# Kernel optimization log

Measured on AMD Instinct MI355X. Metric: run time of the kernel, lower is better.

The kernel has to match this reference:

```python
import jax, jax.numpy as jnp
import numpy as np

B, C, H, W = 8, 512, 32, 32
S, E = 77, 768
NH = 8
HD = C // NH
HID = 4 * C
EPS2D = 1e-6
EPS_QK = 1.1920929e-07  # torch nn.RMSNorm default eps = fp32 machine eps


def rotate_half(x):
    p = x.reshape(*x.shape[:-1], -1, 2)
    p = jnp.stack([-p[..., 1], p[..., 0]], axis=-1)
    return p.reshape(x.shape)


def rope_1d(x):
    # x: [B, NH, S, HD] -- standard 1D RoPE over the sequence axis
    d = x.shape[-1]
    inv_freq = 1.0 / (10000.0 ** (jnp.arange(0, d, 2, dtype=jnp.float32) / d))
    ang = jnp.arange(x.shape[-2], dtype=jnp.float32)[:, None] * inv_freq[None, :]  # [S, HD/2]
    cos = jnp.repeat(jnp.cos(ang), 2, axis=-1)
    sin = jnp.repeat(jnp.sin(ang), 2, axis=-1)
    return x * cos + rotate_half(x) * sin


def rope_2d(x, freqs, h, w):
    # x: [B, NH, H*W, HD]; freqs: [HD/2, 2] learned (theta_y, theta_x)
    gy, gx = jnp.meshgrid(jnp.arange(h, dtype=jnp.float32), jnp.arange(w, dtype=jnp.float32), indexing='ij')
    ang = gy.reshape(-1)[:, None] * freqs[None, :, 0] + gx.reshape(-1)[:, None] * freqs[None, :, 1]  # [HW, HD/2]
    cos = jnp.repeat(jnp.cos(ang), 2, axis=-1)
    sin = jnp.repeat(jnp.sin(ang), 2, axis=-1)
    return x * cos + rotate_half(x) * sin


def rmsnorm_last(x, wgt, eps):
    return x * jax.lax.rsqrt(jnp.mean(x * x, axis=-1, keepdims=True) + eps) * wgt


def rmsnorm_2d(x, wgt):
    # x: [B,C,H,W], RMS over channel dim (dim=1)
    return x * jax.lax.rsqrt(jnp.mean(x * x, axis=1, keepdims=True) + EPS2D) * wgt[None, :, None, None]


def setup_inputs() -> dict:
    key = jax.random.key(0)
    ks = jax.random.split(key, 12)

    def n(k, shp, s=0.02):
        return jax.random.normal(k, shp, jnp.float32) * s

    return {
        'x': jax.random.normal(ks[0], (B, C, H, W), jnp.float32),
        'cond_seq': jax.random.normal(ks[1], (B, S, E), jnp.float32),
        'final_emb': jax.random.normal(ks[2], (B, E), jnp.float32),
        'mod_w': n(ks[3], (E, 6 * C)),
        'mod_b': jnp.zeros((6 * C,), jnp.float32),
        'norm1_scale': jnp.ones((C,), jnp.float32),
        'norm2_scale': jnp.ones((C,), jnp.float32),
        'qkv_s_w': n(ks[4], (3 * C, C)),
        'qkv_c_w': n(ks[5], (3 * C, E)),
        'rope_freqs': jax.random.normal(ks[6], (HD // 2, 2), jnp.float32),
        'qn_w': jnp.ones((HD,), jnp.float32),
        'kn_w': jnp.ones((HD,), jnp.float32),
        'out_w': n(ks[7], (C, C)),
        'out_b': jnp.zeros((C,), jnp.float32),
        'mlp_w1': n(ks[8], (HID, C)),
        'mlp_b1': jnp.zeros((HID,), jnp.float32),
        'mlp_w2': n(ks[9], (C, HID)),
        'mlp_b2': jnp.zeros((C,), jnp.float32),
    }


def reference(x, cond_seq, final_emb, mod_w, mod_b, norm1_scale, norm2_scale,
              qkv_s_w, qkv_c_w, rope_freqs, qn_w, kn_w, out_w, out_b,
              mlp_w1, mlp_b1, mlp_w2, mlp_b2):
    b, c, h, w = x.shape
    hw = h * w
    # adaLN modulation (Modulation: SiLU -> Linear -> 6 chunks)
    mod = jax.nn.silu(final_emb) @ mod_w + mod_b  # [B, 6C]
    sh1, sc1, g1, sh2, sc2, g2 = jnp.split(mod, 6, axis=-1)

    def modulate(z, shift, scale):
        return z * (1.0 + scale[:, :, None, None]) + shift[:, :, None, None]

    h_mod = modulate(rmsnorm_2d(x, norm1_scale), sh1, sc1)

    # --- FusedAttentionBlock: dual-stream (spatial + conditional) attention ---
    hm = h_mod.reshape(b, c, hw)
    qkv_s = jnp.einsum('bcn,oc->bon', hm, qkv_s_w)  # 1x1 conv, [B,3C,HW]
    q_s, k_s, v_s = jnp.split(qkv_s, 3, axis=1)

    def to_heads(t):  # [B,C,HW] -> [B,NH,HW,HD] (head-major channel layout)
        return t.reshape(b, NH, HD, hw).transpose(0, 1, 3, 2)

    q_s, k_s, v_s = to_heads(q_s), to_heads(k_s), to_heads(v_s)

    qkv_c = jnp.einsum('bse,oe->bso', cond_seq, qkv_c_w)
    qkv_c = qkv_c.reshape(b, -1, 3, NH, HD).transpose(2, 0, 3, 1, 4)
    q_c, k_c, v_c = qkv_c[0], qkv_c[1], qkv_c[2]  # [B,NH,S,HD]

    q = jnp.concatenate([rope_2d(q_s, rope_freqs, h, w), rope_1d(q_c)], axis=2)
    k = jnp.concatenate([rope_2d(k_s, rope_freqs, h, w), rope_1d(k_c)], axis=2)
    v = jnp.concatenate([v_s, v_c], axis=2)

    q = rmsnorm_last(q, qn_w, EPS_QK)
    k = rmsnorm_last(k, kn_w, EPS_QK)

    scale = 1.0 / (HD ** 0.5)
    logits = jnp.einsum('bhqd,bhkd->bhqk', q, k) * scale
    attn = jax.nn.softmax(logits, axis=-1)
    o = jnp.einsum('bhqk,bhkd->bhqd', attn, v)[:, :, :hw, :]  # spatial stream only
    o = o.transpose(0, 2, 1, 3).reshape(b, hw, c)
    o = jnp.einsum('bnc,oc->bno', o, out_w) + out_b
    attn_out = o.transpose(0, 2, 1).reshape(b, c, h, w)

    x = x + g1[:, :, None, None] * attn_out

    # --- MLP (1x1 convs, tanh-approx GELU) ---
    h2 = modulate(rmsnorm_2d(x, norm2_scale), sh2, sc2)
    m = jnp.einsum('bchw,oc->bohw', h2, mlp_w1) + mlp_b1[None, :, None, None]
    m = jax.nn.gelu(m, approximate=True)
    m = jnp.einsum('bchw,oc->bohw', m, mlp_w2) + mlp_b2[None, :, None, None]
    return x + g2[:, :, None, None] * m
```

## Files before the change

kernel.cpp:

```cpp
#include <hip/hip_runtime.h>

constexpr int BATCH = 8, CH = 512, HWN = 1024, SEQ = 77, EMB = 768;
constexpr int NHEAD = 8, HDIM = 64, HIDDEN = 2048, TTOT = 1101;
constexpr int VSTRIDE = 1152;

typedef short bhalf8 __attribute__((ext_vector_type(8)));
typedef float f32x4 __attribute__((ext_vector_type(4)));

__device__ __forceinline__ unsigned short f2bf(float f) {
    unsigned u = __builtin_bit_cast(unsigned, f);
    unsigned r = (u + 0x7fffu + ((u >> 16) & 1u)) >> 16;
    return (unsigned short)r;
}
__device__ __forceinline__ unsigned cvtpk(float a, float b) {
    unsigned r;
    asm("v_cvt_pk_bf16_f32 %0, %1, %2" : "=v"(r) : "v"(a), "v"(b));
    return r;
}
__device__ __forceinline__ float gelu_tanh(float v) {
    float c = v * v * v;
    float t = tanhf(0.7978845608028654f * (v + 0.044715f * c));
    return 0.5f * v * (1.0f + t);
}
__device__ __forceinline__ int swz(int b) { return b ^ ((b >> 3) & 0x70); }

__device__ __forceinline__ void gload16(const void* g, void* l) {
    __builtin_amdgcn_global_load_lds(
        (const __attribute__((address_space(1))) unsigned int*)g,
        (__attribute__((address_space(3))) unsigned int*)l, 16, 0, 0);
}

struct PrepArgs {
    const float* src[6];
    unsigned short* dst[6];
    int n[6];
    const float* freqs;
    float* ct;
    const float* emb;
    const float* mbias;
    float* mod;
    float* se;
    const float* qn;
    const float* kn;
    float* mbound;
};
__global__ void k_prep(PrepArgs a) {
    int y = blockIdx.y;
    int bx = blockIdx.x;
    int tid = threadIdx.x;
    if (y < 6) {
        int i = (bx * 256 + tid) * 4;
        if (i >= a.n[y]) return;
        float4 v = *(const float4*)&a.src[y][i];
        ushort4 o = {f2bf(v.x), f2bf(v.y), f2bf(v.z), f2bf(v.w)};
        *(ushort4*)&a.dst[y][i] = o;
    } else if (y == 6) {
        int i = bx * 256 + tid;
        if (i >= TTOT * 32) return;
        int t = i >> 5, j = i & 31;
        float ang;
        if (t < HWN) {
            ang = (float)(t >> 5) * a.freqs[2 * j] + (float)(t & 31) * a.freqs[2 * j + 1];
        } else {
            float inv = expf(-(float)j * (9.210340371976184f / 32.0f));
            ang = (float)(t - HWN) * inv;
        }
        a.ct[i * 2] = cosf(ang);
        a.ct[i * 2 + 1] = sinf(ang);
    } else {
        if (bx < 24) {
            int i = bx * 1024 + tid * 4;
            int j = i - (i / (6 * CH)) * (6 * CH);
            *(float4*)&a.mod[i] = *(const float4*)&a.mbias[j];
        } else if (bx == 24) {
            if (tid < 64) {
                float mq = fabsf(a.qn[tid]), mk = fabsf(a.kn[tid]);
                #pragma unroll
                for (int o = 1; o < 64; o <<= 1) {
                    mq = fmaxf(mq, __shfl_xor(mq, o));
                    mk = fmaxf(mk, __shfl_xor(mk, o));
                }
                if (tid == 0) a.mbound[0] = 64.0f * mq * mk * 0.18033688011112042f + 1.0f;
            }
        } else if (bx >= 32 && bx < 38) {
            int i = (bx - 32) * 1024 + tid * 4;
            float4 v = *(const float4*)&a.emb[i];
            float4 o;
            o.x = v.x / (1.0f + expf(-v.x));
            o.y = v.y / (1.0f + expf(-v.y));
            o.z = v.z / (1.0f + expf(-v.z));
            o.w = v.w / (1.0f + expf(-v.w));
            *(float4*)&a.se[i] = o;
        }
    }
}

__global__ __launch_bounds__(256) void k_mod(const float* __restrict__ se,
        const float* __restrict__ w, float* __restrict__ mod) {
    int jb = blockIdx.x, b = blockIdx.y, ec = blockIdx.z;
    int j = jb * 256 + threadIdx.x;
    const float* sb = se + b * EMB + ec * 96;
    const float* wb = w + (size_t)(ec * 96) * (6 * CH) + j;
    float acc = 0.f;
    #pragma unroll 8
    for (int e = 0; e < 96; ++e) acc = fmaf(sb[e], wb[(size_t)e * (6 * CH)], acc);
    atomicAdd(&mod[b * (6 * CH) + j], acc);
}

__global__ __launch_bounds__(256) void k_rms2d_mod_t(const float* __restrict__ xin,
        const float* __restrict__ sw, const float* __restrict__ mod, int shoff, int scoff,
        unsigned short* __restrict__ outp) {
    __shared__ float part[4][64];
    __shared__ float rinv[64];
    int b = blockIdx.y;
    int n0 = blockIdx.x * 64;
    int tid = threadIdx.x;
    const float* xb = xin + (size_t)b * CH * HWN;
    {
        int n = n0 + (tid & 63);
        int cg = tid >> 6;
        float ss = 0.f;
        #pragma unroll 8
        for (int c = cg * 128; c < cg * 128 + 128; ++c) {
            float v = xb[(size_t)c * HWN + n];
            ss = fmaf(v, v, ss);
        }
        part[cg][tid & 63] = ss;
    }
    __syncthreads();
    if (tid < 64) {
        float s = part[0][tid] + part[1][tid] + part[2][tid] + part[3][tid];
        rinv[tid] = rsqrtf(s * (1.0f / CH) + 1e-6f);
    }
    __syncthreads();
    int n = n0 + (tid >> 2);
    int cq = tid & 3;
    float r = rinv[tid >> 2];
    const float* mb = mod + b * (6 * CH);
    unsigned short* orow = outp + ((size_t)(b * HWN + n)) * CH;
    for (int jc = 0; jc < 16; ++jc) {
        int c = cq * 128 + jc * 8;
        bhalf8 o;
        #pragma unroll
        for (int u = 0; u < 8; ++u) {
            int cc = c + u;
            float v = xb[(size_t)cc * HWN + n];
            float y = v * r * sw[cc] * (1.0f + mb[scoff + cc]) + mb[shoff + cc];
            o[u] = (short)f2bf(y);
        }
        *(bhalf8*)&orow[c] = o;
    }
}

template <int EPI, int BM, int BN>
__global__ __launch_bounds__(256) void k_gemm_mfma(
        const unsigned short* __restrict__ A, const unsigned short* __restrict__ Bt,
        void* __restrict__ OutV, int M, int N, int K,
        const float* __restrict__ bias, const float* __restrict__ gate,
        const float* __restrict__ res) {
    constexpr int WM = BM / 2, WN = BN / 2;
    constexpr int MI = WM / 16, NI = WN / 16;
    constexpr int CA = BM / 8, CB = BN / 8, CW = (CA + CB) / 4;
    constexpr int BUF = (BM + BN) * 128;
    __shared__ __align__(1024) char SM[2 * BUF];
    int tid = threadIdx.x;
    int w = tid >> 6, l = tid & 63, lg = l >> 4, ll = l & 15;
    int wr = w >> 1, wc = w & 1;
    int m0 = blockIdx.y * BM, n0 = blockIdx.x * BN;
    int r8 = l >> 3, c16 = (l & 7) * 16;
    f32x4 acc[MI][NI] = {};
    const char* Ac = (const char*)A;
    const char* Bc = (const char*)Bt;
    size_t rowBytes = (size_t)K * 2;
    int nt = K >> 6;

    auto stage = [&](int t, int bsel) {
        char* As = SM + bsel * BUF;
        char* Bs = As + BM * 128;
        int k0 = t * 64;
        #pragma unroll
        for (int i = 0; i < CW; ++i) {
            int c = w * CW + i;
            if (c < CA) {
                int row = c * 8 + r8;
                int off = c16 ^ ((row & 7) << 4);
                int ar = m0 + row;
                if (ar > M - 1) ar = M - 1;
                gload16(Ac + (size_t)ar * rowBytes + k0 * 2 + off, As + c * 1024);
            } else {
                int cc = c - CA;
                int row = cc * 8 + r8;
                int off = c16 ^ ((row & 7) << 4);
                gload16(Bc + (size_t)(n0 + row) * rowBytes + k0 * 2 + off, Bs + cc * 1024);
            }
        }
    };
    stage(0, 0);
    __syncthreads();
    for (int t = 0; t < nt; ++t) {
        int cur = t & 1;
        if (t + 1 < nt) stage(t + 1, cur ^ 1);
        char* As = SM + cur * BUF;
        char* Bs = As + BM * 128;
        #pragma unroll
        for (int ks = 0; ks < 2; ++ks) {
            bhalf8 af[MI], bf[NI];
            #pragma unroll
            for (int mi = 0; mi < MI; ++mi)
                af[mi] = *(const bhalf8*)(As + swz((wr * WM + mi * 16 + ll) * 128 + ks * 64 + lg * 16));
            #pragma unroll
            for (int ni = 0; ni < NI; ++ni)
                bf[ni] = *(const bhalf8*)(Bs + swz((wc * WN + ni * 16 + ll) * 128 + ks * 64 + lg * 16));
            __builtin_amdgcn_s_setprio(1);
            #pragma unroll
            for (int mi = 0; mi < MI; ++mi)
                #pragma unroll
                for (int ni = 0; ni < NI; ++ni)
                    acc[mi][ni] = __builtin_amdgcn_mfma_f32_16x16x32_bf16(af[mi], bf[ni], acc[mi][ni], 0, 0, 0);
            __builtin_amdgcn_s_setprio(0);
        }
        __syncthreads();
    }
    if (EPI == 2) {
        unsigned short* Out = (unsigned short*)OutV;
        #pragma unroll
        for (int mi = 0; mi < MI; ++mi)
            #pragma unroll
            for (int ni = 0; ni < NI; ++ni) {
                int col = n0 + wc * WN + ni * 16 + ll;
                float bv = bias[col];
                #pragma unroll
                for (int r = 0; r < 4; ++r) {
                    int mrow = m0 + wr * WM + mi * 16 + 4 * lg + r;
                    Out[(size_t)mrow * N + col] = f2bf(gelu_tanh(acc[mi][ni][r] + bv));
                }
            }
    } else {
        float* Out = (float*)OutV;
        int bidx = m0 >> 10;
        int hw0 = m0 & 1023;
        const float* resb = res + (size_t)bidx * N * HWN;
        float* outb_ = Out + (size_t)bidx * N * HWN;
        #pragma unroll
        for (int ni = 0; ni < NI; ++ni) {
            int ch = n0 + wc * WN + ni * 16 + ll;
            float g = gate[bidx * (6 * CH) + ch];
            float bv = bias[ch];
            #pragma unroll
            for (int mi = 0; mi < MI; ++mi) {
                int t = hw0 + wr * WM + mi * 16 + 4 * lg;
                float4 r4 = *(const float4*)&resb[(size_t)ch * HWN + t];
                f32x4 a = acc[mi][ni];
                float4 o;
                o.x = r4.x + g * (a[0] + bv);
                o.y = r4.y + g * (a[1] + bv);
                o.z = r4.z + g * (a[2] + bv);
                o.w = r4.w + g * (a[3] + bv);
                *(float4*)&outb_[(size_t)ch * HWN + t] = o;
            }
        }
    }
}

template <int COND>
__global__ __launch_bounds__(256) void k_gemm_qkv(
        const unsigned short* __restrict__ A, const unsigned short* __restrict__ Bt,
        int M, int K, int nOff, const float* __restrict__ ct,
        const float* __restrict__ qn, const float* __restrict__ kn,
        unsigned short* __restrict__ qb, unsigned short* __restrict__ kb,
        unsigned short* __restrict__ vT) {
    __shared__ __align__(1024) char SMEM[34816];
    unsigned short* As = (unsigned short*)SMEM;
    unsigned short* Bs = (unsigned short*)(SMEM + 16384);
    int tid = threadIdx.x;
    int w = tid >> 6, l = tid & 63, lg = l >> 4, ll = l & 15;
    int wr = w >> 1, wc = w & 1;
    int m0 = blockIdx.y * 128, n0 = nOff + blockIdx.x * 128;
    int r8 = l >> 3, c16 = (l & 7) * 16;
    f32x4 acc[4][4] = {};
    const char* Ac = (const char*)A;
    const char* Bc = (const char*)Bt;
    size_t rowBytes = (size_t)K * 2;
    for (int k0 = 0; k0 < K; k0 += 64) {
        __syncthreads();
        #pragma unroll
        for (int i = 0; i < 8; ++i) {
            int c = w * 8 + i;
            if (c < 16) {
                int row = c * 8 + r8;
                int off = c16 ^ ((row & 7) << 4);
                int ar = m0 + row;
                if (ar > M - 1) ar = M - 1;
                gload16(Ac + (size_t)ar * rowBytes + k0 * 2 + off, (char*)As + c * 1024);
            } else {
                int cc = c - 16;
                int row = cc * 8 + r8;
                int off = c16 ^ ((row & 7) << 4);
                gload16(Bc + (size_t)(n0 + row) * rowBytes + k0 * 2 + off, (char*)Bs + cc * 1024);
            }
        }
        __syncthreads();
        #pragma unroll
        for (int ks = 0; ks < 2; ++ks) {
            bhalf8 af[4], bf[4];
            #pragma unroll
            for (int mi = 0; mi < 4; ++mi)
                af[mi] = *(const bhalf8*)((char*)As + swz((wr * 64 + mi * 16 + ll) * 128 + ks * 64 + lg * 16));
            #pragma unroll
            for (int ni = 0; ni < 4; ++ni)
                bf[ni] = *(const bhalf8*)((char*)Bs + swz((wc * 64 + ni * 16 + ll) * 128 + ks * 64 + lg * 16));
            __builtin_amdgcn_s_setprio(1);
            #pragma unroll
            for (int mi = 0; mi < 4; ++mi)
                #pragma unroll
                for (int ni = 0; ni < 4; ++ni)
                    acc[mi][ni] = __builtin_amdgcn_mfma_f32_16x16x32_bf16(af[mi], bf[ni], acc[mi][ni], 0, 0, 0);
            __builtin_amdgcn_s_setprio(0);
        }
    }
    int type = n0 >> 9;
    const float2* ct2 = (const float2*)ct;

    if (type >= 2) {
        int hd = (n0 - 1024 + wc * 64) >> 6;
        #pragma unroll
        for (int ni = 0; ni < 4; ++ni) {
            int d = ni * 16 + ll;
            #pragma unroll
            for (int mi = 0; mi < 4; ++mi) {
                int rowL = m0 + wr * 64 + mi * 16 + 4 * lg;
                if (COND == 0) {
                    int b = rowL >> 10, t = rowL & 1023;
                    uint2 pk = {cvtpk(acc[mi][ni][0], acc[mi][ni][1]),
                                cvtpk(acc[mi][ni][2], acc[mi][ni][3])};
                    *(uint2*)&vT[((size_t)(b * 8 + hd) * 64 + d) * VSTRIDE + t] = pk;
                } else {
                    #pragma unroll
                    for (int r = 0; r < 4; ++r) {
                        int row = rowL + r;
                        if (row < M) {
                            int b = row / 77, s = row - b * 77;
                            vT[((size_t)(b * 8 + hd) * 64 + d) * VSTRIDE + 1024 + s] =
                                f2bf(acc[mi][ni][r]);
                        }
                    }
                }
            }
        }
        return;
    }
    const float* wnt = (type == 0) ? qn : kn;
    float wn[4];
    int jj[4];
    #pragma unroll
    for (int ni = 0; ni < 4; ++ni) {
        wn[ni] = wnt[ni * 16 + ll];
        jj[ni] = (ni * 16 + ll) >> 1;
    }
    float sgn = (ll & 1) ? 1.f : -1.f;
    #pragma unroll
    for (int mi = 0; mi < 4; ++mi) {
        int rowL = m0 + wr * 64 + mi * 16 + 4 * lg;
        int tt[4];
        #pragma unroll
        for (int r = 0; r < 4; ++r) {
            if (COND == 0) tt[r] = (rowL + r) & 1023;
            else {
                int row = rowL + r;
                if (row > M - 1) row = M - 1;
                int b = row / 77;
                tt[r] = 1024 + (row - b * 77);
            }
        }
        #pragma unroll
        for (int ni = 0; ni < 4; ++ni) {
            f32x4 a = acc[mi][ni], p;
            #pragma unroll
            for (int r = 0; r < 4; ++r) p[r] = __shfl_xor(a[r], 1);
            #pragma unroll
            for (int r = 0; r < 4; ++r) {
                float2 cs = ct2[tt[r] * 32 + jj[ni]];
                a[r] = fmaf(sgn * p[r], cs.y, a[r] * cs.x);
            }
            acc[mi][ni] = a;
        }
        f32x4 ss = {};
        #pragma unroll
        for (int ni = 0; ni < 4; ++ni)
            #pragma unroll
            for (int r = 0; r < 4; ++r) ss[r] = fmaf(acc[mi][ni][r], acc[mi][ni][r], ss[r]);
        #pragma unroll
        for (int msk = 1; msk < 16; msk <<= 1)
            #pragma unroll
            for (int r = 0; r < 4; ++r) ss[r] += __shfl_xor(ss[r], msk);
        f32x4 ri;
        #pragma unroll
        for (int r = 0; r < 4; ++r) {
            ri[r] = rsqrtf(ss[r] * (1.0f / 64.f) + 1.1920929e-07f);
            if (type == 0) ri[r] *= 0.18033688011112042f;
        }
        #pragma unroll
        for (int ni = 0; ni < 4; ++ni)
            #pragma unroll
            for (int r = 0; r < 4; ++r) acc[mi][ni][r] *= ri[r] * wn[ni];
    }
    __syncthreads();
    unsigned short* stg = (unsigned short*)SMEM;
    #pragma unroll
    for (int mi = 0; mi < 4; ++mi)
        #pragma unroll
        for (int ni = 0; ni < 4; ++ni) {
            int colL = wc * 64 + ni * 16 + ll;
            int rowL = wr * 64 + mi * 16 + 4 * lg;
            #pragma unroll
            for (int r = 0; r < 4; ++r)
                stg[(rowL + r) * 136 + colL] = f2bf(acc[mi][ni][r]);
        }
    __syncthreads();
    int rowO = tid >> 1, half = tid & 1;
    int rowG = m0 + rowO;
    if (COND == 1 && rowG >= M) return;
    int ch0 = n0 + half * 64;
    int b, t;
    if (COND == 0) { b = rowG >> 10; t = rowG & 1023; }
    else { b = rowG / 77; t = 1024 + (rowG - b * 77); }
    unsigned short* dst;
    if (type == 0) dst = qb + ((size_t)(b * 8 + (ch0 >> 6)) * HWN + t) * 64;
    else dst = kb + ((size_t)(b * 8 + ((ch0 - 512) >> 6)) * TTOT + t) * 64;
    #pragma unroll
    for (int i = 0; i < 8; ++i)
        *(bhalf8*)&dst[i * 8] = *(const bhalf8*)&stg[rowO * 136 + half * 64 + i * 8];
}

__global__ __launch_bounds__(256) void k_attn_v7(const unsigned short* __restrict__ qb,
        const unsigned short* __restrict__ kbuf, const unsigned short* __restrict__ vT,
        unsigned short* __restrict__ ob, const float* __restrict__ mbp) {
    __shared__ __align__(1024) char smc[40960];
    int f = blockIdx.x;
    int xcd = f & 7, n = f >> 3;
    int q0 = (n & 15) * 64;
    int bh = ((n >> 4) << 3) | xcd;
    int tid = threadIdx.x;
    int w = tid >> 6, l = tid & 63, lg = l >> 4, ll = l & 15;
    int r8 = l >> 3, c16 = (l & 7) * 16;
    float Mb = mbp[0];
    bhalf8 qf[2];
    {
        const unsigned short* qbase = qb + ((size_t)bh * HWN + q0 + w * 16) * 64;
        #pragma unroll
        for (int ks = 0; ks < 2; ++ks)
            qf[ks] = *(const bhalf8*)&qbase[ll * 64 + ks * 32 + lg * 8];
    }
    f32x4 accO[4] = {};
    float Lx = 0.f;
    const char* kgl = (const char*)kbuf + (size_t)bh * TTOT * 128;
    const char* vgl = (const char*)vT + (size_t)bh * 64 * (VSTRIDE * 2);
    char* pw = smc + 32768 + w * 2048 + ll * 128;
    int pswz = (ll & 7) << 4;

    auto stage = [&](int kt, int bsel) {
        char* base = smc + bsel * 16384;
        #pragma unroll
        for (int i = 0; i < 4; ++i) {
            int c = w * 4 + i;
            if (c < 8) {
                int row = c * 8 + r8;
                int t = kt * 64 + row;
                if (t > TTOT - 1) t = TTOT - 1;
                gload16(kgl + (size_t)t * 128 + (c16 ^ ((row & 7) << 4)), base + c * 1024);
            } else {
                int row = (c - 8) * 8 + r8;
                gload16(vgl + (size_t)row * (VSTRIDE * 2) + kt * 128 + (c16 ^ ((row & 7) << 4)),
                        base + 8192 + (c - 8) * 1024);
            }
        }
    };
    stage(0, 0);
    __syncthreads();
    for (int kt = 0; kt < 18; ++kt) {
        int cur = kt & 1;
        if (kt < 17) stage(kt + 1, cur ^ 1);
        char* kl = smc + cur * 16384;
        char* vl = kl + 8192;
        f32x4 s[4] = {};
        __builtin_amdgcn_s_setprio(1);
        #pragma unroll
        for (int ks = 0; ks < 2; ++ks) {
            bhalf8 kf[4];
            #pragma unroll
            for (int k4 = 0; k4 < 4; ++k4)
                kf[k4] = *(const bhalf8*)(kl + swz((k4 * 16 + ll) * 128 + ks * 64 + lg * 16));
            #pragma unroll
            for (int k4 = 0; k4 < 4; ++k4)
                s[k4] = __builtin_amdgcn_mfma_f32_16x16x32_bf16(kf[k4], qf[ks], s[k4], 0, 0, 0);
        }
        __builtin_amdgcn_s_setprio(0);
        if (kt == 17) {
            int kb0 = kt * 64 + 4 * lg;
            #pragma unroll
            for (int k4 = 0; k4 < 4; ++k4)
                #pragma unroll
                for (int r = 0; r < 4; ++r)
                    if (kb0 + k4 * 16 + r >= TTOT) s[k4][r] = -1e30f;
        }
        float sum = 0.f;
        #pragma unroll
        for (int k4 = 0; k4 < 4; ++k4) {
            float p0 = exp2f(s[k4][0] - Mb), p1 = exp2f(s[k4][1] - Mb);
            float p2 = exp2f(s[k4][2] - Mb), p3 = exp2f(s[k4][3] - Mb);
            sum += (p0 + p1) + (p2 + p3);
            uint2 pk = {cvtpk(p0, p1), cvtpk(p2, p3)};
            *(uint2*)(pw + ((k4 * 32 + lg * 8) ^ pswz)) = pk;
        }
        sum += __shfl_xor(sum, 16);
        sum += __shfl_xor(sum, 32);
        Lx += sum;
        __builtin_amdgcn_s_setprio(1);
        #pragma unroll
        for (int ks = 0; ks < 2; ++ks) {
            bhalf8 vf[4];
            #pragma unroll
            for (int d4 = 0; d4 < 4; ++d4)
                vf[d4] = *(const bhalf8*)(vl + swz((d4 * 16 + ll) * 128 + ks * 64 + lg * 16));
            bhalf8 pf = *(const bhalf8*)(smc + 32768 + w * 2048 + swz(ll * 128 + ks * 64 + lg * 16));
            #pragma unroll
            for (int d4 = 0; d4 < 4; ++d4)
                accO[d4] = __builtin_amdgcn_mfma_f32_16x16x32_bf16(vf[d4], pf, accO[d4], 0, 0, 0);
        }
        __builtin_amdgcn_s_setprio(0);
        __syncthreads();
    }
    {
        float inv = 1.0f / Lx;
        int orow = w * 16 + ll;
        char* po = smc + orow * 128;
        int oswz = (orow & 7) << 4;
        #pragma unroll
        for (int d4 = 0; d4 < 4; ++d4) {
            uint2 pk = {cvtpk(accO[d4][0] * inv, accO[d4][1] * inv),
                        cvtpk(accO[d4][2] * inv, accO[d4][3] * inv)};
            *(uint2*)(po + ((d4 * 32 + lg * 8) ^ oswz)) = pk;
        }
    }
    __syncthreads();
    int b = bh >> 3, h = bh & 7;
    int row = tid >> 2, seg = tid & 3;
    bhalf8 v0 = *(const bhalf8*)(smc + swz(row * 128 + seg * 32));
    bhalf8 v1 = *(const bhalf8*)(smc + swz(row * 128 + seg * 32 + 16));
    unsigned short* dst = ob + ((size_t)(b * HWN + q0 + row)) * CH + h * 64 + seg * 16;
    *(bhalf8*)&dst[0] = v0;
    *(bhalf8*)&dst[8] = v1;
}

extern "C" void kernel_launch(void* const* d_in, const int* in_sizes, int n_in,
                              void* d_out, int out_size, void* d_ws, size_t ws_size,
                              hipStream_t stream) {
    const float* x     = (const float*)d_in[0];
    const float* cond  = (const float*)d_in[1];
    const float* femb  = (const float*)d_in[2];
    const float* mod_w = (const float*)d_in[3];
    const float* mod_b = (const float*)d_in[4];
    const float* n1s   = (const float*)d_in[5];
    const float* n2s   = (const float*)d_in[6];
    const float* qkvsw = (const float*)d_in[7];
    const float* qkvcw = (const float*)d_in[8];
    const float* ropef = (const float*)d_in[9];
    const float* qn    = (const float*)d_in[10];
    const float* kn    = (const float*)d_in[11];
    const float* outw  = (const float*)d_in[12];
    const float* outb  = (const float*)d_in[13];
    const float* w1    = (const float*)d_in[14];
    const float* b1    = (const float*)d_in[15];
    const float* w2    = (const float*)d_in[16];
    const float* b2    = (const float*)d_in[17];
    float* out = (float*)d_out;
    char* W = (char*)d_ws;

    unsigned short* wqs_b = (unsigned short*)(W + 0);
    unsigned short* wqc_b = (unsigned short*)(W + 1572864);
    unsigned short* wo_b  = (unsigned short*)(W + 3932160);
    unsigned short* w1_b  = (unsigned short*)(W + 4456448);
    unsigned short* w2_b  = (unsigned short*)(W + 6553600);
    unsigned short* condb = (unsigned short*)(W + 8650752);
    float* mod            = (float*)(W + 9596928);
    float* ct             = (float*)(W + 9695232);
    unsigned short* hmod  = (unsigned short*)(W + 9977088);
    unsigned short* obuf  = hmod;
    unsigned short* qbuf  = (unsigned short*)(W + 18365696);
    unsigned short* kbuf  = (unsigned short*)(W + 26754304);
    unsigned short* vTb   = (unsigned short*)(W + 35772672);
    unsigned short* h2    = vTb;
    unsigned short* mbuf  = (unsigned short*)(W + 45209856);
    float* x1             = (float*)(W + 78764288);
    float* mbound         = (float*)(W + 45209856);
    float* sebuf          = (float*)(W + 45209920);

    PrepArgs pa;
    pa.src[0] = qkvsw; pa.dst[0] = wqs_b; pa.n[0] = 1536 * 512;
    pa.src[1] = qkvcw; pa.dst[1] = wqc_b; pa.n[1] = 1536 * 768;
    pa.src[2] = outw;  pa.dst[2] = wo_b;  pa.n[2] = 512 * 512;
    pa.src[3] = w1;    pa.dst[3] = w1_b;  pa.n[3] = 2048 * 512;
    pa.src[4] = w2;    pa.dst[4] = w2_b;  pa.n[4] = 512 * 2048;
    pa.src[5] = cond;  pa.dst[5] = condb; pa.n[5] = 616 * 768;
    pa.freqs = ropef; pa.ct = ct;
    pa.emb = femb; pa.mbias = mod_b; pa.mod = mod; pa.se = sebuf;
    pa.qn = qn; pa.kn = kn; pa.mbound = mbound;
    k_prep<<<dim3(1152, 8), 256, 0, stream>>>(pa);
    k_mod<<<dim3(12, 8, 8), 256, 0, stream>>>(sebuf, mod_w, mod);

    k_rms2d_mod_t<<<dim3(16, BATCH), 256, 0, stream>>>(x, n1s, mod, 0, 512, hmod);
    k_gemm_qkv<0><<<dim3(12, 64), 256, 0, stream>>>(hmod, wqs_b, 8192, 512, 0,
                                                    ct, qn, kn, qbuf, kbuf, vTb);
    k_gemm_qkv<1><<<dim3(8, 5), 256, 0, stream>>>(condb, wqc_b, 616, 768, 512,
                                                  ct, qn, kn, qbuf, kbuf, vTb);
    k_attn_v7<<<dim3(1024), 256, 0, stream>>>(qbuf, kbuf, vTb, obuf, mbound);
    k_gemm_mfma<1, 128, 64><<<dim3(8, 64), 256, 0, stream>>>(
        obuf, wo_b, x1, 8192, 512, 512, outb, mod + 2 * 512, x);
    k_rms2d_mod_t<<<dim3(16, BATCH), 256, 0, stream>>>(x1, n2s, mod, 3 * 512, 4 * 512, h2);
    k_gemm_mfma<2, 64, 128><<<dim3(16, 128), 256, 0, stream>>>(
        h2, w1_b, mbuf, 8192, 2048, 512, b1, nullptr, nullptr);
    k_gemm_mfma<1, 128, 64><<<dim3(8, 64), 256, 0, stream>>>(
        mbuf, w2_b, out, 8192, 512, 2048, b2, mod + 5 * 512, x1);
}
```

Before: 269.3 us.

## Triple-buffer GEMM loads and compute attention row sums with an MFMA

```diff
diff --git a/kernel.cpp b/kernel.cpp
--- a/kernel.cpp
+++ b/kernel.cpp
@@ -40,9 +40,6 @@
     const float* mbias;
     float* mod;
     float* se;
-    const float* qn;
-    const float* kn;
-    float* mbound;
 };
 __global__ void k_prep(PrepArgs a) {
     int y = blockIdx.y;
@@ -72,16 +69,6 @@
             int i = bx * 1024 + tid * 4;
             int j = i - (i / (6 * CH)) * (6 * CH);
             *(float4*)&a.mod[i] = *(const float4*)&a.mbias[j];
-        } else if (bx == 24) {
-            if (tid < 64) {
-                float mq = fabsf(a.qn[tid]), mk = fabsf(a.kn[tid]);
-                #pragma unroll
-                for (int o = 1; o < 64; o <<= 1) {
-                    mq = fmaxf(mq, __shfl_xor(mq, o));
-                    mk = fmaxf(mk, __shfl_xor(mk, o));
-                }
-                if (tid == 0) a.mbound[0] = 64.0f * mq * mk * 0.18033688011112042f + 1.0f;
-            }
         } else if (bx >= 32 && bx < 38) {
             int i = (bx - 32) * 1024 + tid * 4;
             float4 v = *(const float4*)&a.emb[i];
@@ -162,7 +149,9 @@
     constexpr int MI = WM / 16, NI = WN / 16;
     constexpr int CA = BM / 8, CB = BN / 8, CW = (CA + CB) / 4;
     constexpr int BUF = (BM + BN) * 128;
-    __shared__ __align__(1024) char SM[2 * BUF];
+    constexpr unsigned WAIT_CW = (CW & 0xF) | ((CW >> 4) << 14) | (0x7 << 4) | (0xF << 8);
+    constexpr unsigned WAIT_0 = (0x7 << 4) | (0xF << 8);
+    __shared__ __align__(1024) char SM[3 * BUF];
     int tid = threadIdx.x;
     int w = tid >> 6, l = tid & 63, lg = l >> 4, ll = l & 15;
     int wr = w >> 1, wc = w & 1;
@@ -196,10 +185,14 @@
         }
     };
     stage(0, 0);
-    __syncthreads();
+    stage(1, 1);
+    int cur = 0;
     for (int t = 0; t < nt; ++t) {
-        int cur = t & 1;
-        if (t + 1 < nt) stage(t + 1, cur ^ 1);
+        if (t + 1 < nt) __builtin_amdgcn_s_waitcnt(WAIT_CW);
+        else __builtin_amdgcn_s_waitcnt(WAIT_0);
+        __builtin_amdgcn_s_barrier();
+        __builtin_amdgcn_sched_barrier(0);
+        if (t + 2 < nt) stage(t + 2, (cur + 2) % 3);
         char* As = SM + cur * BUF;
         char* Bs = As + BM * 128;
         #pragma unroll
@@ -219,7 +212,8 @@
                     acc[mi][ni] = __builtin_amdgcn_mfma_f32_16x16x32_bf16(af[mi], bf[ni], acc[mi][ni], 0, 0, 0);
             __builtin_amdgcn_s_setprio(0);
         }
-        __syncthreads();
+        __builtin_amdgcn_sched_barrier(0);
+        cur = (cur + 1) % 3;
     }
     if (EPI == 2) {
         unsigned short* Out = (unsigned short*)OutV;
@@ -432,9 +426,9 @@
         *(bhalf8*)&dst[i * 8] = *(const bhalf8*)&stg[rowO * 136 + half * 64 + i * 8];
 }
 
-__global__ __launch_bounds__(256) void k_attn_v7(const unsigned short* __restrict__ qb,
+__global__ __launch_bounds__(256) void k_attn_v8(const unsigned short* __restrict__ qb,
         const unsigned short* __restrict__ kbuf, const unsigned short* __restrict__ vT,
-        unsigned short* __restrict__ ob, const float* __restrict__ mbp) {
+        unsigned short* __restrict__ ob) {
     __shared__ __align__(1024) char smc[40960];
     int f = blockIdx.x;
     int xcd = f & 7, n = f >> 3;
@@ -443,7 +437,6 @@
     int tid = threadIdx.x;
     int w = tid >> 6, l = tid & 63, lg = l >> 4, ll = l & 15;
     int r8 = l >> 3, c16 = (l & 7) * 16;
-    float Mb = mbp[0];
     bhalf8 qf[2];
     {
         const unsigned short* qbase = qb + ((size_t)bh * HWN + q0 + w * 16) * 64;
@@ -451,8 +444,11 @@
         for (int ks = 0; ks < 2; ++ks)
             qf[ks] = *(const bhalf8*)&qbase[ll * 64 + ks * 32 + lg * 8];
     }
+    bhalf8 onesf;
+    #pragma unroll
+    for (int i = 0; i < 8; ++i) onesf[i] = (short)0x3F80;
     f32x4 accO[4] = {};
-    float Lx = 0.f;
+    f32x4 Lacc = {};
     const char* kgl = (const char*)kbuf + (size_t)bh * TTOT * 128;
     const char* vgl = (const char*)vT + (size_t)bh * 64 * (VSTRIDE * 2);
     char* pw = smc + 32768 + w * 2048 + ll * 128;
@@ -503,18 +499,13 @@
                 for (int r = 0; r < 4; ++r)
                     if (kb0 + k4 * 16 + r >= TTOT) s[k4][r] = -1e30f;
         }
-        float sum = 0.f;
         #pragma unroll
         for (int k4 = 0; k4 < 4; ++k4) {
-            float p0 = exp2f(s[k4][0] - Mb), p1 = exp2f(s[k4][1] - Mb);
-            float p2 = exp2f(s[k4][2] - Mb), p3 = exp2f(s[k4][3] - Mb);
-            sum += (p0 + p1) + (p2 + p3);
+            float p0 = exp2f(s[k4][0]), p1 = exp2f(s[k4][1]);
+            float p2 = exp2f(s[k4][2]), p3 = exp2f(s[k4][3]);
             uint2 pk = {cvtpk(p0, p1), cvtpk(p2, p3)};
             *(uint2*)(pw + ((k4 * 32 + lg * 8) ^ pswz)) = pk;
         }
-        sum += __shfl_xor(sum, 16);
-        sum += __shfl_xor(sum, 32);
-        Lx += sum;
         __builtin_amdgcn_s_setprio(1);
         #pragma unroll
         for (int ks = 0; ks < 2; ++ks) {
@@ -523,6 +514,7 @@
             for (int d4 = 0; d4 < 4; ++d4)
                 vf[d4] = *(const bhalf8*)(vl + swz((d4 * 16 + ll) * 128 + ks * 64 + lg * 16));
             bhalf8 pf = *(const bhalf8*)(smc + 32768 + w * 2048 + swz(ll * 128 + ks * 64 + lg * 16));
+            Lacc = __builtin_amdgcn_mfma_f32_16x16x32_bf16(onesf, pf, Lacc, 0, 0, 0);
             #pragma unroll
             for (int d4 = 0; d4 < 4; ++d4)
                 accO[d4] = __builtin_amdgcn_mfma_f32_16x16x32_bf16(vf[d4], pf, accO[d4], 0, 0, 0);
@@ -531,7 +523,7 @@
         __syncthreads();
     }
     {
-        float inv = 1.0f / Lx;
+        float inv = 1.0f / Lacc[0];
         int orow = w * 16 + ll;
         char* po = smc + orow * 128;
         int oswz = (orow & 7) << 4;
@@ -592,7 +584,6 @@
     unsigned short* h2    = vTb;
     unsigned short* mbuf  = (unsigned short*)(W + 45209856);
     float* x1             = (float*)(W + 78764288);
-    float* mbound         = (float*)(W + 45209856);
     float* sebuf          = (float*)(W + 45209920);
 
     PrepArgs pa;
@@ -604,7 +595,6 @@
     pa.src[5] = cond;  pa.dst[5] = condb; pa.n[5] = 616 * 768;
     pa.freqs = ropef; pa.ct = ct;
     pa.emb = femb; pa.mbias = mod_b; pa.mod = mod; pa.se = sebuf;
-    pa.qn = qn; pa.kn = kn; pa.mbound = mbound;
     k_prep<<<dim3(1152, 8), 256, 0, stream>>>(pa);
     k_mod<<<dim3(12, 8, 8), 256, 0, stream>>>(sebuf, mod_w, mod);
 
@@ -613,7 +603,7 @@
                                                     ct, qn, kn, qbuf, kbuf, vTb);
     k_gemm_qkv<1><<<dim3(8, 5), 256, 0, stream>>>(condb, wqc_b, 616, 768, 512,
                                                   ct, qn, kn, qbuf, kbuf, vTb);
-    k_attn_v7<<<dim3(1024), 256, 0, stream>>>(qbuf, kbuf, vTb, obuf, mbound);
+    k_attn_v8<<<dim3(1024), 256, 0, stream>>>(qbuf, kbuf, vTb, obuf);
     k_gemm_mfma<1, 128, 64><<<dim3(8, 64), 256, 0, stream>>>(
         obuf, wo_b, x1, 8192, 512, 512, outb, mod + 2 * 512, x);
     k_rms2d_mod_t<<<dim3(16, BATCH), 256, 0, stream>>>(x1, n2s, mod, 3 * 512, 4 * 512, h2);
```

Measured after the change: 269.5 us. No clear change (+0.1%).
